# Performance work log

Hardware: AMD Instinct MI355X
Metric: run time of the kernel (lower is better)

The kernel has to match this reference:

```python
import jax, jax.numpy as jnp
import numpy as np

N = 50000          # nodes
E = 800000         # directed edges (avg degree 16)
IN_F = 1433        # Cora num_features
N_CLS = 7          # Cora num_classes
HEADS = 8
HID = 32
NEG_SLOPE = 0.2    # PyG GATConv default negative_slope


def gat_conv(x, src, dst, W, a_src, a_dst, bias, heads, out_ch):
    """PyG GATConv (concat=True, add_self_loops=True, eval mode)."""
    n = x.shape[0]
    h = (x @ W).reshape(n, heads, out_ch)            # [N, H, C]
    # add self loops (PyG default)
    loop = jnp.arange(n, dtype=src.dtype)
    src = jnp.concatenate([src, loop])
    dst = jnp.concatenate([dst, loop])
    # attention logits per edge: a_src . h_src + a_dst . h_dst
    alpha_src = (h * a_src).sum(-1)                  # [N, H]
    alpha_dst = (h * a_dst).sum(-1)                  # [N, H]
    e = jax.nn.leaky_relu(alpha_src[src] + alpha_dst[dst], NEG_SLOPE)  # [E+N, H]
    # segment softmax over incoming edges of each destination node
    m = jax.ops.segment_max(e, dst, num_segments=n)  # [N, H]
    p = jnp.exp(e - m[dst])
    denom = jax.ops.segment_sum(p, dst, num_segments=n)
    alpha = p / denom[dst]                           # [E+N, H]
    # attention-weighted scatter-aggregate of source features
    out = jax.ops.segment_sum(h[src] * alpha[:, :, None], dst, num_segments=n)  # [N, H, C]
    return out.reshape(n, heads * out_ch) + bias


def setup_inputs() -> dict:
    key = jax.random.key(0)
    ks = jax.random.split(key, 12)
    s = 0.05
    x = jax.random.normal(ks[0], (N, IN_F), dtype=jnp.float32)
    edge_index = jax.random.randint(ks[1], (2, E), 0, N, dtype=jnp.int32)
    W1 = jax.random.normal(ks[2], (IN_F, HEADS * HID), dtype=jnp.float32) * s
    att_src1 = jax.random.normal(ks[3], (HEADS, HID), dtype=jnp.float32) * s
    att_dst1 = jax.random.normal(ks[4], (HEADS, HID), dtype=jnp.float32) * s
    bias1 = jnp.zeros((HEADS * HID,), dtype=jnp.float32)
    W2 = jax.random.normal(ks[5], (HEADS * HID, HEADS * N_CLS), dtype=jnp.float32) * s
    att_src2 = jax.random.normal(ks[6], (HEADS, N_CLS), dtype=jnp.float32) * s
    att_dst2 = jax.random.normal(ks[7], (HEADS, N_CLS), dtype=jnp.float32) * s
    bias2 = jnp.zeros((HEADS * N_CLS,), dtype=jnp.float32)
    return {
        "x": x, "edge_index": edge_index,
        "W1": W1, "att_src1": att_src1, "att_dst1": att_dst1, "bias1": bias1,
        "W2": W2, "att_src2": att_src2, "att_dst2": att_dst2, "bias2": bias2,
    }


def reference(x, edge_index, W1, att_src1, att_dst1, bias1,
              W2, att_src2, att_dst2, bias2):
    src, dst = edge_index[0], edge_index[1]
    # dropout (p=0.6) is identity in eval mode
    h = gat_conv(x, src, dst, W1, att_src1, att_dst1, bias1, HEADS, HID)
    h = jax.nn.elu(h)
    out = gat_conv(h, src, dst, W2, att_src2, att_dst2, bias2, HEADS, N_CLS)
    return out  # [N, HEADS * N_CLS]
```

## Files before the change

kernel.cpp:

```cpp
#include <hip/hip_runtime.h>
#include <math.h>

typedef short s16x8 __attribute__((ext_vector_type(8)));
typedef float f32x4 __attribute__((ext_vector_type(4)));

#define SLOPE 0.2f
#define K1 1433
#define KP 1440
#define NKB 45

static __device__ __forceinline__ float leaky(float x) {
  return x > 0.f ? x : SLOPE * x;
}

static __device__ __forceinline__ unsigned short f2bf(float f) {
  unsigned u = __builtin_bit_cast(unsigned, f);
  u += 0x7FFFu + ((u >> 16) & 1u);
  return (unsigned short)(u >> 16);
}
static __device__ __forceinline__ float bf2f(unsigned short h) {
  unsigned u = ((unsigned)h) << 16;
  return __builtin_bit_cast(float, u);
}

__global__ void w1t_kernel(const float* __restrict__ W1,
                           unsigned short* __restrict__ w1f) {
  int tid = blockIdx.x * 256 + threadIdx.x;
  if (tid >= NKB * 16 * 64) return;
  int l = tid & 63;
  int chunk = tid >> 6;
  int ntg = chunk & 15;
  int kb = chunk >> 4;
  int n = ntg * 16 + (l & 15);
  int kbase = kb * 32 + (l >> 4) * 8;
  unsigned short o[8];
#pragma unroll
  for (int e = 0; e < 8; ++e) {
    int k = kbase + e;
    float v = (k < K1) ? W1[(long)k * 256 + n] : 0.f;
    o[e] = f2bf(v);
  }
  *(ulonglong2*)(w1f + (long)tid * 8) = *(ulonglong2*)o;
}

__global__ __launch_bounds__(256, 3) void gemm1_mfma_kernel(
    const float* __restrict__ A, const unsigned short* __restrict__ w1f,
    float* __restrict__ C, int M) {
  __shared__ unsigned short Bs[2][16 * 64 * 8];
  const int t = threadIdx.x;
  const int w = t >> 6, l = t & 63;
  const int wm = w >> 1, wn = w & 1;
  const int row0 = blockIdx.x * 64;
  const int lrow = l & 15, lkg = l >> 4;

  f32x4 acc[2][8];
#pragma unroll
  for (int mt = 0; mt < 2; ++mt)
#pragma unroll
    for (int nt = 0; nt < 8; ++nt)
#pragma unroll
      for (int r = 0; r < 4; ++r) acc[mt][nt][r] = 0.f;

  const int r0 = row0 + wm * 32 + lrow;
  const int r1 = r0 + 16;
  const bool ok0 = r0 < M, ok1 = r1 < M;
  const float* a0 = A + (long)(ok0 ? r0 : 0) * K1 + lkg * 8;
  const float* a1 = A + (long)(ok1 ? r1 : 0) * K1 + lkg * 8;
  const float4 f4z = make_float4(0.f, 0.f, 0.f, 0.f);

  auto stage = [&](int kb, int buf) {
#pragma unroll
    for (int q = 0; q < 4; ++q) {
      int ng = w * 4 + q;
      const unsigned short* gsrc = w1f + (((long)kb * 16 + ng) * 64 + l) * 8;
      unsigned short* ldst = &Bs[buf][ng * 512];
      __builtin_amdgcn_global_load_lds(
          (const __attribute__((address_space(1))) unsigned int*)gsrc,
          (__attribute__((address_space(3))) unsigned int*)ldst, 16, 0, 0);
    }
  };

  auto loada = [&](int kb, float4* v) {
    if (kb < NKB - 1) {
      v[0] = ok0 ? *(const float4*)(a0 + kb * 32) : f4z;
      v[1] = ok0 ? *(const float4*)(a0 + kb * 32 + 4) : f4z;
      v[2] = ok1 ? *(const float4*)(a1 + kb * 32) : f4z;
      v[3] = ok1 ? *(const float4*)(a1 + kb * 32 + 4) : f4z;
    } else {
      if (lkg < 3) {
        v[0] = ok0 ? *(const float4*)(a0 + kb * 32) : f4z;
        v[1] = ok0 ? *(const float4*)(a0 + kb * 32 + 4) : f4z;
        v[2] = ok1 ? *(const float4*)(a1 + kb * 32) : f4z;
        v[3] = ok1 ? *(const float4*)(a1 + kb * 32 + 4) : f4z;
      } else {
        v[0] = f4z; v[1] = f4z; v[2] = f4z; v[3] = f4z;
        v[0].x = ok0 ? a0[kb * 32] : 0.f;
        v[2].x = ok1 ? a1[kb * 32] : 0.f;
      }
    }
  };

  auto cvt2 = [&](const float4& x, const float4& y, s16x8& ah, s16x8& al) {
    float f[8] = {x.x, x.y, x.z, x.w, y.x, y.y, y.z, y.w};
#pragma unroll
    for (int e = 0; e < 8; ++e) {
      unsigned short h = f2bf(f[e]);
      ah[e] = (short)h;
      al[e] = (short)f2bf(f[e] - bf2f(h));
    }
  };

  auto compute = [&](int cur, const float4* v) {
    s16x8 ah0, al0, ah1, al1;
    cvt2(v[0], v[1], ah0, al0);
    cvt2(v[2], v[3], ah1, al1);
    const unsigned short* bp = &Bs[cur][wn * 8 * 512 + l * 8];
#pragma unroll
    for (int nt = 0; nt < 8; ++nt) {
      s16x8 bh = *(const s16x8*)(bp + nt * 512);
      acc[0][nt] = __builtin_amdgcn_mfma_f32_16x16x32_bf16(ah0, bh, acc[0][nt], 0, 0, 0);
      acc[0][nt] = __builtin_amdgcn_mfma_f32_16x16x32_bf16(al0, bh, acc[0][nt], 0, 0, 0);
      acc[1][nt] = __builtin_amdgcn_mfma_f32_16x16x32_bf16(ah1, bh, acc[1][nt], 0, 0, 0);
      acc[1][nt] = __builtin_amdgcn_mfma_f32_16x16x32_bf16(al1, bh, acc[1][nt], 0, 0, 0);
    }
  };

  float4 vA[4], vB[4];
  stage(0, 0);
  loada(0, vA);
  __syncthreads();

  for (int kb = 0; kb < NKB - 1; kb += 2) {
    stage(kb + 1, 1);
    loada(kb + 1, vB);
    compute(0, vA);
    __syncthreads();
    if (kb + 2 < NKB) {
      stage(kb + 2, 0);
      loada(kb + 2, vA);
    }
    compute(1, vB);
    __syncthreads();
  }
  compute(0, vA);

  const int crow4 = (l >> 4) * 4;
#pragma unroll
  for (int mt = 0; mt < 2; ++mt) {
#pragma unroll
    for (int r = 0; r < 4; ++r) {
      int grow = row0 + wm * 32 + mt * 16 + crow4 + r;
      if (grow < M) {
#pragma unroll
        for (int nt = 0; nt < 8; ++nt) {
          int gcol = wn * 128 + nt * 16 + lrow;
          C[(long)grow * 256 + gcol] = acc[mt][nt][r];
        }
      }
    }
  }
}

__global__ void alpha1_kernel(const float* __restrict__ h1,
    const float* __restrict__ a_src, const float* __restrict__ a_dst,
    float* __restrict__ as_o, float* __restrict__ ad_o,
    unsigned short* __restrict__ h1b, int N) {
  int i = blockIdx.x * blockDim.x + threadIdx.x;
  if (i >= N * 8) return;
  int h = i & 7;
  const float* hp = h1 + (long)(i >> 3) * 256 + h * 32;
  const float* sp = a_src + h * 32;
  const float* dp = a_dst + h * 32;
  unsigned short ob[32];
  float s1 = 0.f, s2 = 0.f;
#pragma unroll
  for (int c = 0; c < 32; c += 4) {
    float4 v = *(const float4*)(hp + c);
    float4 ws = *(const float4*)(sp + c);
    float4 wd = *(const float4*)(dp + c);
    s1 += v.x * ws.x + v.y * ws.y + v.z * ws.z + v.w * ws.w;
    s2 += v.x * wd.x + v.y * wd.y + v.z * wd.z + v.w * wd.w;
    ob[c] = f2bf(v.x); ob[c + 1] = f2bf(v.y);
    ob[c + 2] = f2bf(v.z); ob[c + 3] = f2bf(v.w);
  }
  as_o[i] = s1;
  ad_o[i] = s2;
  unsigned short* op = h1b + (long)(i >> 3) * 256 + h * 32;
#pragma unroll
  for (int c = 0; c < 32; c += 8)
    *(ulonglong2*)(op + c) = *(ulonglong2*)(ob + c);
}

__global__ void hist_kernel(const int* __restrict__ dst, int* __restrict__ cnt,
                            int E, int N) {
  int e = blockIdx.x * blockDim.x + threadIdx.x;
  if (e >= E + N) return;
  int d = (e < E) ? dst[e] : (e - E);
  atomicAdd(&cnt[d], 1);
}

__global__ __launch_bounds__(1024) void scan_kernel(
    const int* __restrict__ cnt, int* __restrict__ rowptr,
    int* __restrict__ cursor, int N) {
  __shared__ int part[1024];
  const int tid = threadIdx.x;
  const int chunk = (N + 1023) / 1024;
  const int base = tid * chunk;
  const int lim = min(base + chunk, N);
  int sum = 0;
  for (int i = base; i < lim; ++i) sum += cnt[i];
  part[tid] = sum;
  __syncthreads();
  for (int off = 1; off < 1024; off <<= 1) {
    int v = (tid >= off) ? part[tid - off] : 0;
    __syncthreads();
    part[tid] += v;
    __syncthreads();
  }
  int run = (tid == 0) ? 0 : part[tid - 1];
  for (int i = base; i < lim; ++i) {
    rowptr[i] = run;
    cursor[i] = run;
    run += cnt[i];
  }
  if (tid == 1023) rowptr[N] = part[1023];
}

__global__ void scatter_kernel(const int* __restrict__ src,
    const int* __restrict__ dst, int* __restrict__ cursor,
    int* __restrict__ csr_src, int E, int N) {
  int e = blockIdx.x * blockDim.x + threadIdx.x;
  if (e >= E + N) return;
  int s, d;
  if (e < E) { s = src[e]; d = dst[e]; } else { s = e - E; d = s; }
  int pos = atomicAdd(&cursor[d], 1);
  csr_src[pos] = s;
}

__global__ __launch_bounds__(256) void agg1_fused_kernel(
    const int* __restrict__ rowptr, const int* __restrict__ csr_src,
    const float* __restrict__ as_, const float* __restrict__ ad_,
    const unsigned short* __restrict__ h1b, const float* __restrict__ bias,
    float* __restrict__ act, int N) {
  int d = blockIdx.x * 4 + (threadIdx.x >> 6);
  if (d >= N) return;
  int l = threadIdx.x & 63;
  int h = l >> 3;
  int rs = rowptr[d], re = rowptr[d + 1];
  float adv = ad_[d * 8 + h];
  float4 acc = make_float4(0.f, 0.f, 0.f, 0.f);
  float den = 0.f;
  int sN = csr_src[rs];
  float asN = as_[sN * 8 + h];
  for (int i = rs; i < re; ++i) {
    int sC = sN;
    float asC = asN;
    if (i + 1 < re) {
      sN = csr_src[i + 1];
      asN = as_[sN * 8 + h];
    }
    float a = __expf(leaky(asC + adv));
    ushort4 u = *(const ushort4*)(h1b + (long)sC * 256 + l * 4);
    den += a;
    acc.x += a * bf2f(u.x); acc.y += a * bf2f(u.y);
    acc.z += a * bf2f(u.z); acc.w += a * bf2f(u.w);
  }
  float inv = 1.f / den;
  float4 b = *(const float4*)(bias + l * 4);
  float4 o;
  o.x = acc.x * inv + b.x; o.y = acc.y * inv + b.y;
  o.z = acc.z * inv + b.z; o.w = acc.w * inv + b.w;
  o.x = o.x > 0.f ? o.x : expm1f(o.x);
  o.y = o.y > 0.f ? o.y : expm1f(o.y);
  o.z = o.z > 0.f ? o.z : expm1f(o.z);
  o.w = o.w > 0.f ? o.w : expm1f(o.w);
  *(float4*)(act + (long)d * 256 + l * 4) = o;
}

__global__ __launch_bounds__(256) void gemm2_kernel(const float* __restrict__ act,
    const float* __restrict__ W2, const float* __restrict__ a_src2,
    const float* __restrict__ a_dst2, unsigned short* __restrict__ h2b,
    float* __restrict__ as_o, float* __restrict__ ad_o, int N) {
  __shared__ float Ws[256 * 56];
  for (int i = threadIdx.x; i < 256 * 56; i += 256) Ws[i] = W2[i];
  __syncthreads();
  int n = blockIdx.x * 32 + (threadIdx.x >> 3);
  int h = threadIdx.x & 7;
  if (n >= N) return;
  const float* ap = act + (long)n * 256;
  float acc[7] = {0.f, 0.f, 0.f, 0.f, 0.f, 0.f, 0.f};
  for (int k0 = 0; k0 < 256; k0 += 4) {
    float4 a = *(const float4*)(ap + k0);
    float av[4] = {a.x, a.y, a.z, a.w};
#pragma unroll
    for (int kk = 0; kk < 4; ++kk) {
      const float* wp = &Ws[(k0 + kk) * 56 + h * 7];
#pragma unroll
      for (int j = 0; j < 7; ++j) acc[j] += av[kk] * wp[j];
    }
  }
  unsigned short* hp = h2b + (long)n * 56 + h * 7;
  float s1 = 0.f, s2 = 0.f;
#pragma unroll
  for (int j = 0; j < 7; ++j) {
    hp[j] = f2bf(acc[j]);
    s1 += acc[j] * a_src2[h * 7 + j];
    s2 += acc[j] * a_dst2[h * 7 + j];
  }
  as_o[n * 8 + h] = s1;
  ad_o[n * 8 + h] = s2;
}

__global__ __launch_bounds__(256) void agg2_fused_kernel(
    const int* __restrict__ rowptr, const int* __restrict__ csr_src,
    const float* __restrict__ as_, const float* __restrict__ ad_,
    const unsigned short* __restrict__ h2b, const float* __restrict__ bias,
    float* __restrict__ out, int N) {
  int d = blockIdx.x * 4 + (threadIdx.x >> 6);
  if (d >= N) return;
  int l = threadIdx.x & 63;
  int h = l >> 3, j = l & 7;
  int rs = rowptr[d], re = rowptr[d + 1];
  float adv = ad_[d * 8 + h];
  float acc = 0.f, den = 0.f;
  int sN = csr_src[rs];
  float asN = as_[sN * 8 + h];
  for (int i = rs; i < re; ++i) {
    int sC = sN;
    float asC = asN;
    if (i + 1 < re) {
      sN = csr_src[i + 1];
      asN = as_[sN * 8 + h];
    }
    float a = __expf(leaky(asC + adv));
    den += a;
    if (j < 7) acc += a * bf2f(h2b[(long)sC * 56 + h * 7 + j]);
  }
  if (j < 7) out[(long)d * 56 + h * 7 + j] = acc / den + bias[h * 7 + j];
}

extern "C" void kernel_launch(void* const* d_in, const int* in_sizes, int n_in,
                              void* d_out, int out_size, void* d_ws, size_t ws_size,
                              hipStream_t stream) {
  const float* x    = (const float*)d_in[0];
  const int*   ei   = (const int*)d_in[1];
  const float* W1   = (const float*)d_in[2];
  const float* asr1 = (const float*)d_in[3];
  const float* adt1 = (const float*)d_in[4];
  const float* b1   = (const float*)d_in[5];
  const float* W2   = (const float*)d_in[6];
  const float* asr2 = (const float*)d_in[7];
  const float* adt2 = (const float*)d_in[8];
  const float* b2   = (const float*)d_in[9];
  float* out = (float*)d_out;

  const int N = in_sizes[0] / K1;
  const int E = in_sizes[1] / 2;
  const int* src = ei;
  const int* dst = ei + E;

  float* ws = (float*)d_ws;
  float* h1  = ws; ws += (long)N * 256;
  float* act = ws; ws += (long)N * 256;
  float* as1 = ws; ws += N * 8;
  float* ad1 = ws; ws += N * 8;
  float* as2 = ws; ws += N * 8;
  float* ad2 = ws; ws += N * 8;
  unsigned short* h1b = (unsigned short*)ws; ws += (long)N * 128;
  unsigned short* h2b = (unsigned short*)ws; ws += (long)N * 28;
  unsigned short* w1f = (unsigned short*)ws; ws += NKB * 16 * 64 * 8 / 2;
  int* cnt     = (int*)ws; ws += N;
  int* rowptr  = (int*)ws; ws += N + 1;
  int* cursor  = (int*)ws; ws += N;
  int* csr_src = (int*)ws; ws += E + N;

  hipMemsetAsync(cnt, 0, (size_t)N * sizeof(int), stream);

  dim3 blk(256);

  hist_kernel<<<dim3((E + N + 255) / 256), blk, 0, stream>>>(dst, cnt, E, N);
  scan_kernel<<<dim3(1), dim3(1024), 0, stream>>>(cnt, rowptr, cursor, N);
  scatter_kernel<<<dim3((E + N + 255) / 256), blk, 0, stream>>>(
      src, dst, cursor, csr_src, E, N);
  {
    int tot = NKB * 16 * 64;
    w1t_kernel<<<dim3((tot + 255) / 256), blk, 0, stream>>>(W1, w1f);
  }

  gemm1_mfma_kernel<<<dim3((N + 63) / 64), blk, 0, stream>>>(x, w1f, h1, N);
  alpha1_kernel<<<dim3((N * 8 + 255) / 256), blk, 0, stream>>>(
      h1, asr1, adt1, as1, ad1, h1b, N);
  agg1_fused_kernel<<<dim3((N + 3) / 4), blk, 0, stream>>>(
      rowptr, csr_src, as1, ad1, h1b, b1, act, N);
  gemm2_kernel<<<dim3((N + 31) / 32), blk, 0, stream>>>(
      act, W2, asr2, adt2, h2b, as2, ad2, N);
  agg2_fused_kernel<<<dim3((N + 3) / 4), blk, 0, stream>>>(
      rowptr, csr_src, as2, ad2, h2b, b2, out, N);
}
```

Measured before the change: 805.7 us.

## Load GEMM1 B fragments directly to registers, emit bf16 h1, pad h2 rows

GEMM1 drops LDS staging and block barriers and instead loads pre-swizzled W1 fragments from global memory straight into registers, with double-buffered register prefetch. Its launch bound falls from 3 to 2 waves per SIMD to make room for the extra registers. GEMM1 now writes bf16 h1 directly, so the fp32 h1 buffer and the conversion in alpha1 go away and alpha1 reads bf16 input. The layer-2 features are padded to 8 per head so agg2 loads without a mod-7 index. This trades the LDS sharing of B across waves for more global/L2 traffic, and computes the attention logits from bf16-rounded h1.

```diff
diff --git a/kernel.cpp b/kernel.cpp
--- a/kernel.cpp
+++ b/kernel.cpp
@@ -29,9 +29,9 @@
   if (tid >= NKB * 16 * 64) return;
   int l = tid & 63;
   int chunk = tid >> 6;
-  int ntg = chunk & 15;
+  int ng = chunk & 15;
   int kb = chunk >> 4;
-  int n = ntg * 16 + (l & 15);
+  int n = ng * 16 + (l & 15);
   int kbase = kb * 32 + (l >> 4) * 8;
   unsigned short o[8];
 #pragma unroll
@@ -43,10 +43,9 @@
   *(ulonglong2*)(w1f + (long)tid * 8) = *(ulonglong2*)o;
 }
 
-__global__ __launch_bounds__(256, 3) void gemm1_mfma_kernel(
+__global__ __launch_bounds__(256, 2) void gemm1_mfma_kernel(
     const float* __restrict__ A, const unsigned short* __restrict__ w1f,
-    float* __restrict__ C, int M) {
-  __shared__ unsigned short Bs[2][16 * 64 * 8];
+    unsigned short* __restrict__ h1b, int M) {
   const int t = threadIdx.x;
   const int w = t >> 6, l = t & 63;
   const int wm = w >> 1, wn = w & 1;
@@ -68,19 +67,7 @@
   const float* a1 = A + (long)(ok1 ? r1 : 0) * K1 + lkg * 8;
   const float4 f4z = make_float4(0.f, 0.f, 0.f, 0.f);
 
-  auto stage = [&](int kb, int buf) {
-#pragma unroll
-    for (int q = 0; q < 4; ++q) {
-      int ng = w * 4 + q;
-      const unsigned short* gsrc = w1f + (((long)kb * 16 + ng) * 64 + l) * 8;
-      unsigned short* ldst = &Bs[buf][ng * 512];
-      __builtin_amdgcn_global_load_lds(
-          (const __attribute__((address_space(1))) unsigned int*)gsrc,
-          (__attribute__((address_space(3))) unsigned int*)ldst, 16, 0, 0);
-    }
-  };
-
-  auto loada = [&](int kb, float4* v) {
+  auto la = [&](int kb, float4* v) {
     if (kb < NKB - 1) {
       v[0] = ok0 ? *(const float4*)(a0 + kb * 32) : f4z;
       v[1] = ok0 ? *(const float4*)(a0 + kb * 32 + 4) : f4z;
@@ -100,6 +87,13 @@
     }
   };
 
+  auto lb = [&](int kb, s16x8* b) {
+    const unsigned short* bp = w1f + (((long)kb * 16 + wn * 8) * 64 + l) * 8;
+#pragma unroll
+    for (int nt = 0; nt < 8; ++nt)
+      b[nt] = *(const s16x8*)(bp + nt * 512);
+  };
+
   auto cvt2 = [&](const float4& x, const float4& y, s16x8& ah, s16x8& al) {
     float f[8] = {x.x, x.y, x.z, x.w, y.x, y.y, y.z, y.w};
 #pragma unroll
@@ -110,39 +104,35 @@
     }
   };
 
-  auto compute = [&](int cur, const float4* v) {
+  auto compute = [&](const float4* v, const s16x8* b) {
     s16x8 ah0, al0, ah1, al1;
     cvt2(v[0], v[1], ah0, al0);
     cvt2(v[2], v[3], ah1, al1);
-    const unsigned short* bp = &Bs[cur][wn * 8 * 512 + l * 8];
 #pragma unroll
     for (int nt = 0; nt < 8; ++nt) {
-      s16x8 bh = *(const s16x8*)(bp + nt * 512);
-      acc[0][nt] = __builtin_amdgcn_mfma_f32_16x16x32_bf16(ah0, bh, acc[0][nt], 0, 0, 0);
-      acc[0][nt] = __builtin_amdgcn_mfma_f32_16x16x32_bf16(al0, bh, acc[0][nt], 0, 0, 0);
-      acc[1][nt] = __builtin_amdgcn_mfma_f32_16x16x32_bf16(ah1, bh, acc[1][nt], 0, 0, 0);
-      acc[1][nt] = __builtin_amdgcn_mfma_f32_16x16x32_bf16(al1, bh, acc[1][nt], 0, 0, 0);
+      acc[0][nt] = __builtin_amdgcn_mfma_f32_16x16x32_bf16(ah0, b[nt], acc[0][nt], 0, 0, 0);
+      acc[0][nt] = __builtin_amdgcn_mfma_f32_16x16x32_bf16(al0, b[nt], acc[0][nt], 0, 0, 0);
+      acc[1][nt] = __builtin_amdgcn_mfma_f32_16x16x32_bf16(ah1, b[nt], acc[1][nt], 0, 0, 0);
+      acc[1][nt] = __builtin_amdgcn_mfma_f32_16x16x32_bf16(al1, b[nt], acc[1][nt], 0, 0, 0);
     }
   };
 
-  float4 vA[4], vB[4];
-  stage(0, 0);
-  loada(0, vA);
-  __syncthreads();
-
+  float4 A0[4], A1[4];
+  s16x8 B0[8], B1[8];
+  la(0, A0);
+  la(1, A1);
+  lb(0, B0);
+
+#pragma unroll 1
   for (int kb = 0; kb < NKB - 1; kb += 2) {
-    stage(kb + 1, 1);
-    loada(kb + 1, vB);
-    compute(0, vA);
-    __syncthreads();
-    if (kb + 2 < NKB) {
-      stage(kb + 2, 0);
-      loada(kb + 2, vA);
-    }
-    compute(1, vB);
-    __syncthreads();
-  }
-  compute(0, vA);
+    lb(kb + 1, B1);
+    compute(A0, B0);
+    la(kb + 2, A0);
+    lb(kb + 2 < NKB ? kb + 2 : NKB - 1, B0);
+    compute(A1, B1);
+    la(kb + 3 < NKB ? kb + 3 : NKB - 1, A1);
+  }
+  compute(A0, B0);
 
   const int crow4 = (l >> 4) * 4;
 #pragma unroll
@@ -154,41 +144,34 @@
 #pragma unroll
         for (int nt = 0; nt < 8; ++nt) {
           int gcol = wn * 128 + nt * 16 + lrow;
-          C[(long)grow * 256 + gcol] = acc[mt][nt][r];
+          h1b[(long)grow * 256 + gcol] = f2bf(acc[mt][nt][r]);
         }
       }
     }
   }
 }
 
-__global__ void alpha1_kernel(const float* __restrict__ h1,
+__global__ void alpha1_kernel(const unsigned short* __restrict__ h1b,
     const float* __restrict__ a_src, const float* __restrict__ a_dst,
-    float* __restrict__ as_o, float* __restrict__ ad_o,
-    unsigned short* __restrict__ h1b, int N) {
+    float* __restrict__ as_o, float* __restrict__ ad_o, int N) {
   int i = blockIdx.x * blockDim.x + threadIdx.x;
   if (i >= N * 8) return;
   int h = i & 7;
-  const float* hp = h1 + (long)(i >> 3) * 256 + h * 32;
+  const unsigned short* hp = h1b + (long)(i >> 3) * 256 + h * 32;
   const float* sp = a_src + h * 32;
   const float* dp = a_dst + h * 32;
-  unsigned short ob[32];
   float s1 = 0.f, s2 = 0.f;
 #pragma unroll
   for (int c = 0; c < 32; c += 4) {
-    float4 v = *(const float4*)(hp + c);
+    ushort4 u = *(const ushort4*)(hp + c);
     float4 ws = *(const float4*)(sp + c);
     float4 wd = *(const float4*)(dp + c);
-    s1 += v.x * ws.x + v.y * ws.y + v.z * ws.z + v.w * ws.w;
-    s2 += v.x * wd.x + v.y * wd.y + v.z * wd.z + v.w * wd.w;
-    ob[c] = f2bf(v.x); ob[c + 1] = f2bf(v.y);
-    ob[c + 2] = f2bf(v.z); ob[c + 3] = f2bf(v.w);
+    float vx = bf2f(u.x), vy = bf2f(u.y), vz = bf2f(u.z), vw = bf2f(u.w);
+    s1 += vx * ws.x + vy * ws.y + vz * ws.z + vw * ws.w;
+    s2 += vx * wd.x + vy * wd.y + vz * wd.z + vw * wd.w;
   }
   as_o[i] = s1;
   ad_o[i] = s2;
-  unsigned short* op = h1b + (long)(i >> 3) * 256 + h * 32;
-#pragma unroll
-  for (int c = 0; c < 32; c += 8)
-    *(ulonglong2*)(op + c) = *(ulonglong2*)(ob + c);
 }
 
 __global__ void hist_kernel(const int* __restrict__ dst, int* __restrict__ cnt,
@@ -279,7 +262,7 @@
 
 __global__ __launch_bounds__(256) void gemm2_kernel(const float* __restrict__ act,
     const float* __restrict__ W2, const float* __restrict__ a_src2,
-    const float* __restrict__ a_dst2, unsigned short* __restrict__ h2b,
+    const float* __restrict__ a_dst2, unsigned short* __restrict__ h2p,
     float* __restrict__ as_o, float* __restrict__ ad_o, int N) {
   __shared__ float Ws[256 * 56];
   for (int i = threadIdx.x; i < 256 * 56; i += 256) Ws[i] = W2[i];
@@ -299,14 +282,16 @@
       for (int j = 0; j < 7; ++j) acc[j] += av[kk] * wp[j];
     }
   }
-  unsigned short* hp = h2b + (long)n * 56 + h * 7;
+  unsigned short ob[8];
   float s1 = 0.f, s2 = 0.f;
 #pragma unroll
   for (int j = 0; j < 7; ++j) {
-    hp[j] = f2bf(acc[j]);
+    ob[j] = f2bf(acc[j]);
     s1 += acc[j] * a_src2[h * 7 + j];
     s2 += acc[j] * a_dst2[h * 7 + j];
   }
+  ob[7] = 0;
+  *(ulonglong2*)(h2p + (long)n * 64 + h * 8) = *(ulonglong2*)ob;
   as_o[n * 8 + h] = s1;
   ad_o[n * 8 + h] = s2;
 }
@@ -314,7 +299,7 @@
 __global__ __launch_bounds__(256) void agg2_fused_kernel(
     const int* __restrict__ rowptr, const int* __restrict__ csr_src,
     const float* __restrict__ as_, const float* __restrict__ ad_,
-    const unsigned short* __restrict__ h2b, const float* __restrict__ bias,
+    const unsigned short* __restrict__ h2p, const float* __restrict__ bias,
     float* __restrict__ out, int N) {
   int d = blockIdx.x * 4 + (threadIdx.x >> 6);
   if (d >= N) return;
@@ -334,7 +319,7 @@
     }
     float a = __expf(leaky(asC + adv));
     den += a;
-    if (j < 7) acc += a * bf2f(h2b[(long)sC * 56 + h * 7 + j]);
+    acc += a * bf2f(h2p[(long)sC * 64 + l]);
   }
   if (j < 7) out[(long)d * 56 + h * 7 + j] = acc / den + bias[h * 7 + j];
 }
@@ -360,14 +345,13 @@
   const int* dst = ei + E;
 
   float* ws = (float*)d_ws;
-  float* h1  = ws; ws += (long)N * 256;
   float* act = ws; ws += (long)N * 256;
   float* as1 = ws; ws += N * 8;
   float* ad1 = ws; ws += N * 8;
   float* as2 = ws; ws += N * 8;
   float* ad2 = ws; ws += N * 8;
   unsigned short* h1b = (unsigned short*)ws; ws += (long)N * 128;
-  unsigned short* h2b = (unsigned short*)ws; ws += (long)N * 28;
+  unsigned short* h2p = (unsigned short*)ws; ws += (long)N * 32;
   unsigned short* w1f = (unsigned short*)ws; ws += NKB * 16 * 64 * 8 / 2;
   int* cnt     = (int*)ws; ws += N;
   int* rowptr  = (int*)ws; ws += N + 1;
@@ -387,13 +371,13 @@
     w1t_kernel<<<dim3((tot + 255) / 256), blk, 0, stream>>>(W1, w1f);
   }
 
-  gemm1_mfma_kernel<<<dim3((N + 63) / 64), blk, 0, stream>>>(x, w1f, h1, N);
+  gemm1_mfma_kernel<<<dim3((N + 63) / 64), blk, 0, stream>>>(x, w1f, h1b, N);
   alpha1_kernel<<<dim3((N * 8 + 255) / 256), blk, 0, stream>>>(
-      h1, asr1, adt1, as1, ad1, h1b, N);
+      h1b, asr1, adt1, as1, ad1, N);
   agg1_fused_kernel<<<dim3((N + 3) / 4), blk, 0, stream>>>(
       rowptr, csr_src, as1, ad1, h1b, b1, act, N);
   gemm2_kernel<<<dim3((N + 31) / 32), blk, 0, stream>>>(
-      act, W2, asr2, adt2, h2b, as2, ad2, N);
+      act, W2, asr2, adt2, h2p, as2, ad2, N);
   agg2_fused_kernel<<<dim3((N + 3) / 4), blk, 0, stream>>>(
-      rowptr, csr_src, as2, ad2, h2b, b2, out, N);
-}
+      rowptr, csr_src, as2, ad2, h2p, b2, out, N);
+}
```

Result: faster. 781.5 us (-3.0%).
